# Kernel tuning notes

Hardware: AMD Instinct MI355X
Metric: run time of the kernel (lower is better)

The kernel has to match this reference:

```python
import jax, jax.numpy as jnp
import numpy as np

B, W, H, I, L = 64, 4096, 128, 128, 2


def setup_inputs() -> dict:
    key = jax.random.key(0)
    ks = jax.random.split(key, 16)
    f = lambda k, s: jax.random.normal(k, s, dtype=jnp.float32) * 0.05
    return dict(
        input=f(ks[0], (B, 1, I)),
        h0=f(ks[1], (L, B, H)),
        c0=f(ks[2], (L, B, H)),
        encoder_output=f(ks[3], (B, W, H)),
        att_W=f(ks[4], (1, 2 * H)), att_b=f(ks[5], (1,)),
        inp_W=f(ks[6], (I, H + I)), inp_b=f(ks[7], (I,)),
        W_ih0=f(ks[8], (4 * H, I)), W_hh0=f(ks[9], (4 * H, H)),
        b_ih0=f(ks[10], (4 * H,)), b_hh0=f(ks[11], (4 * H,)),
        W_ih1=f(ks[12], (4 * H, H)), W_hh1=f(ks[13], (4 * H, H)),
        b_ih1=f(ks[14], (4 * H,)), b_hh1=f(ks[15], (4 * H,)),
    )


def _lstm_cell(x, h, c, W_ih, W_hh, b_ih, b_hh):
    # PyTorch gate order: i, f, g, o
    gates = x @ W_ih.T + h @ W_hh.T + b_ih + b_hh
    i, f, g, o = jnp.split(gates, 4, axis=-1)
    c_new = jax.nn.sigmoid(f) * c + jax.nn.sigmoid(i) * jnp.tanh(g)
    h_new = jax.nn.sigmoid(o) * jnp.tanh(c_new)
    return h_new, c_new


def reference(input, h0, c0, encoder_output, att_W, att_b, inp_W, inp_b,
              W_ih0, W_hh0, b_ih0, b_hh0, W_ih1, W_hh1, b_ih1, b_hh1):
    att_state = h0[-1] * c0[-1]                       # (B, H)
    # att_line over concat(enc_word, att_state): split the (1, 2H) weight.
    wa_enc, wa_st = att_W[0, :H], att_W[0, H:]
    scores = encoder_output @ wa_enc + (att_state @ wa_st + att_b[0])[:, None]  # (B, W)
    # Faithful to original: a leading zeros column is prepended, then
    # softmax is taken over [:, 0:-1] -> keeps the zero column, drops the
    # LAST word's score.
    zero_col = jnp.zeros((scores.shape[0], 1), scores.dtype)
    full = jnp.concatenate([zero_col, scores], axis=1)  # (B, W+1)
    weight = jax.nn.softmax(full[:, :-1], axis=1)        # (B, W)
    x = jnp.einsum('bw,bwh->bh', weight, encoder_output)  # (B, H)
    xin = jnp.concatenate([x, input[:, 0, :]], axis=1) @ inp_W.T + inp_b  # (B, I)
    # 2-layer LSTM, single time step (eval mode -> inter-layer dropout off)
    h1, c1 = _lstm_cell(xin, h0[0], c0[0], W_ih0, W_hh0, b_ih0, b_hh0)
    h2, c2 = _lstm_cell(h1, h0[1], c0[1], W_ih1, W_hh1, b_ih1, b_hh1)
    output = h2[:, None, :]                              # (B, 1, H)
    return output, jnp.stack([h1, h2]), jnp.stack([c1, c2])
```

## Files before the change

### kernel.cpp

```cpp
#include <hip/hip_runtime.h>

#define BB 64
#define WW 4096
#define HH 128
#define NCHUNK 32
#define CROWS 128
#define PSTRIDE 132

__device__ inline float sigmoidf(float x) { return 1.0f / (1.0f + expf(-x)); }

__global__ void fused_attention(const float* __restrict__ enc,
                                const float* __restrict__ h0,
                                const float* __restrict__ c0,
                                const float* __restrict__ attW,
                                const float* __restrict__ attb,
                                float* __restrict__ partials) {
    __shared__ float s_wa[128];
    __shared__ float s_red[128];
    __shared__ float s_sc[CROWS];
    __shared__ float racc[16 * 128];
    __shared__ float s_bias, s_m, s_l;

    const int t = threadIdx.x;
    const int b = blockIdx.x >> 5;
    const int chunk = blockIdx.x & 31;
    const int w0 = chunk * CROWS;

    if (t < 128) {
        s_wa[t] = attW[t];
        float hv = h0[BB * HH + b * HH + t];
        float cv = c0[BB * HH + b * HH + t];
        s_red[t] = hv * cv * attW[HH + t];
    }
    __syncthreads();
    for (int s = 64; s > 0; s >>= 1) {
        if (t < s) s_red[t] += s_red[t + s];
        __syncthreads();
    }
    if (t == 0) s_bias = s_red[0] + attb[0];
    __syncthreads();
    const float bias = s_bias;

    const int seg = t & 15;
    const int rg  = t >> 4;
    float wseg[8];
#pragma unroll
    for (int j = 0; j < 8; j++) wseg[j] = s_wa[seg * 8 + j];

#pragma unroll
    for (int pass = 0; pass < 8; pass++) {
        const int r = pass * 16 + rg;
        const size_t w = (size_t)w0 + r;
        const float4* p = (const float4*)(enc + ((size_t)b * WW + w) * HH + seg * 8);
        float4 a = p[0], c = p[1];
        float d = a.x * wseg[0] + a.y * wseg[1] + a.z * wseg[2] + a.w * wseg[3]
                + c.x * wseg[4] + c.y * wseg[5] + c.z * wseg[6] + c.w * wseg[7];
        d += __shfl_xor(d, 8, 16);
        d += __shfl_xor(d, 4, 16);
        d += __shfl_xor(d, 2, 16);
        d += __shfl_xor(d, 1, 16);
        if (seg == 0) s_sc[r] = (w == WW - 1) ? -1e30f : (d + bias);
    }
    __syncthreads();

    if (t < 64) s_red[t] = fmaxf(s_sc[t], s_sc[t + 64]);
    __syncthreads();
    for (int s = 32; s > 0; s >>= 1) {
        if (t < s) s_red[t] = fmaxf(s_red[t], s_red[t + s]);
        __syncthreads();
    }
    if (t == 0) s_m = s_red[0];
    __syncthreads();
    const float m = s_m;

    if (t < 128) s_sc[t] = expf(s_sc[t] - m);
    __syncthreads();
    if (t < 64) s_red[t] = s_sc[t] + s_sc[t + 64];
    __syncthreads();
    for (int s = 32; s > 0; s >>= 1) {
        if (t < s) s_red[t] += s_red[t + s];
        __syncthreads();
    }
    if (t == 0) s_l = s_red[0];

    const int wsub = t >> 4;
    float acc8[8];
#pragma unroll
    for (int j = 0; j < 8; j++) acc8[j] = 0.f;
#pragma unroll
    for (int pass = 0; pass < 8; pass++) {
        const int r = pass * 16 + wsub;
        const size_t w = (size_t)w0 + r;
        if (w + 1 < WW) {
            const float pw = s_sc[r];
            const float4* p = (const float4*)(enc + ((size_t)b * WW + w + 1) * HH + seg * 8);
            float4 a = p[0], c = p[1];
            acc8[0] += pw * a.x; acc8[1] += pw * a.y;
            acc8[2] += pw * a.z; acc8[3] += pw * a.w;
            acc8[4] += pw * c.x; acc8[5] += pw * c.y;
            acc8[6] += pw * c.z; acc8[7] += pw * c.w;
        }
    }
#pragma unroll
    for (int j = 0; j < 8; j++) racc[wsub * 128 + seg * 8 + j] = acc8[j];
    __syncthreads();

    float* out = partials + (size_t)(b * NCHUNK + chunk) * PSTRIDE;
    if (t < 128) {
        float s = 0.f;
#pragma unroll
        for (int w2 = 0; w2 < 16; w2++) s += racc[w2 * 128 + t];
        out[t] = s;
    }
    if (t == 128) out[128] = m;
    if (t == 129) out[129] = s_l;
}

__global__ void tail_kernel(const float* __restrict__ partials,
                            const float* __restrict__ enc,
                            const float* __restrict__ input,
                            const float* __restrict__ inpW,
                            const float* __restrict__ inpb,
                            const float* __restrict__ Wih0,
                            const float* __restrict__ Whh0,
                            const float* __restrict__ bih0,
                            const float* __restrict__ bhh0,
                            const float* __restrict__ Wih1,
                            const float* __restrict__ Whh1,
                            const float* __restrict__ bih1,
                            const float* __restrict__ bhh1,
                            const float* __restrict__ h0,
                            const float* __restrict__ c0,
                            float* __restrict__ out) {
    __shared__ float lm[NCHUNK], llv[NCHUNK], ls[NCHUNK];
    __shared__ float sM, sL;
    __shared__ float xc[256];
    __shared__ float sxv[128];
    __shared__ float shv[128];
    __shared__ float sh1[128];
    __shared__ float shv2[128];
    __shared__ float gates[512];

    const int b = blockIdx.x;
    const int t = threadIdx.x;

    if (t < NCHUNK) {
        const float* pp = partials + (size_t)(b * NCHUNK + t) * PSTRIDE;
        lm[t] = pp[128];
        llv[t] = pp[129];
    }
    __syncthreads();
    if (t == 0) {
        float M = 0.0f;
        for (int c = 0; c < NCHUNK; c++) M = fmaxf(M, lm[c]);
        float L = expf(-M);
        for (int c = 0; c < NCHUNK; c++) {
            float s = expf(lm[c] - M);
            ls[c] = s;
            L += s * llv[c];
        }
        sM = M; sL = L;
    }
    __syncthreads();

    if (t < 128) {
        float xv = expf(-sM) * enc[(size_t)b * WW * HH + t];
        for (int c = 0; c < NCHUNK; c++)
            xv += ls[c] * partials[(size_t)(b * NCHUNK + c) * PSTRIDE + t];
        xc[t] = xv / sL;
        xc[128 + t] = input[b * HH + t];
    }
    __syncthreads();

    if (t < 128) {
        float a = inpb[t];
        const float4* wr = (const float4*)(inpW + (size_t)t * 256);
#pragma unroll
        for (int k = 0; k < 64; k++) {
            float4 w4 = wr[k];
            a += xc[4 * k] * w4.x + xc[4 * k + 1] * w4.y
               + xc[4 * k + 2] * w4.z + xc[4 * k + 3] * w4.w;
        }
        sxv[t] = a;
        shv[t] = h0[b * HH + t];
        shv2[t] = h0[BB * HH + b * HH + t];
    }
    __syncthreads();

    {
        float g = bih0[t] + bhh0[t];
        const float4* wi = (const float4*)(Wih0 + (size_t)t * 128);
        const float4* wh = (const float4*)(Whh0 + (size_t)t * 128);
#pragma unroll
        for (int k = 0; k < 32; k++) {
            float4 a = wi[k], c = wh[k];
            g += sxv[4 * k] * a.x + sxv[4 * k + 1] * a.y + sxv[4 * k + 2] * a.z + sxv[4 * k + 3] * a.w
               + shv[4 * k] * c.x + shv[4 * k + 1] * c.y + shv[4 * k + 2] * c.z + shv[4 * k + 3] * c.w;
        }
        gates[t] = g;
    }
    __syncthreads();
    if (t < 128) {
        float ig = sigmoidf(gates[t]);
        float fg = sigmoidf(gates[128 + t]);
        float gg = tanhf(gates[256 + t]);
        float og = sigmoidf(gates[384 + t]);
        float cn = fg * c0[b * HH + t] + ig * gg;
        float hn = og * tanhf(cn);
        out[8192 + b * HH + t] = hn;
        out[24576 + b * HH + t] = cn;
        sh1[t] = hn;
    }
    __syncthreads();

    {
        float g = bih1[t] + bhh1[t];
        const float4* wi = (const float4*)(Wih1 + (size_t)t * 128);
        const float4* wh = (const float4*)(Whh1 + (size_t)t * 128);
#pragma unroll
        for (int k = 0; k < 32; k++) {
            float4 a = wi[k], c = wh[k];
            g += sh1[4 * k] * a.x + sh1[4 * k + 1] * a.y + sh1[4 * k + 2] * a.z + sh1[4 * k + 3] * a.w
               + shv2[4 * k] * c.x + shv2[4 * k + 1] * c.y + shv2[4 * k + 2] * c.z + shv2[4 * k + 3] * c.w;
        }
        gates[t] = g;
    }
    __syncthreads();
    if (t < 128) {
        float ig = sigmoidf(gates[t]);
        float fg = sigmoidf(gates[128 + t]);
        float gg = tanhf(gates[256 + t]);
        float og = sigmoidf(gates[384 + t]);
        float cn = fg * c0[BB * HH + b * HH + t] + ig * gg;
        float hn = og * tanhf(cn);
        out[b * HH + t] = hn;
        out[16384 + b * HH + t] = hn;
        out[32768 + b * HH + t] = cn;
    }
}

extern "C" void kernel_launch(void* const* d_in, const int* in_sizes, int n_in,
                              void* d_out, int out_size, void* d_ws, size_t ws_size,
                              hipStream_t stream) {
    const float* input = (const float*)d_in[0];
    const float* h0    = (const float*)d_in[1];
    const float* c0    = (const float*)d_in[2];
    const float* enc   = (const float*)d_in[3];
    const float* attW  = (const float*)d_in[4];
    const float* attb  = (const float*)d_in[5];
    const float* inpW  = (const float*)d_in[6];
    const float* inpb  = (const float*)d_in[7];
    const float* Wih0  = (const float*)d_in[8];
    const float* Whh0  = (const float*)d_in[9];
    const float* bih0  = (const float*)d_in[10];
    const float* bhh0  = (const float*)d_in[11];
    const float* Wih1  = (const float*)d_in[12];
    const float* Whh1  = (const float*)d_in[13];
    const float* bih1  = (const float*)d_in[14];
    const float* bhh1  = (const float*)d_in[15];

    float* partials = (float*)d_ws;

    fused_attention<<<BB * NCHUNK, 256, 0, stream>>>(enc, h0, c0, attW, attb, partials);
    tail_kernel<<<BB, 512, 0, stream>>>(partials, enc, input, inpW, inpb,
                                        Wih0, Whh0, bih0, bhh0,
                                        Wih1, Whh1, bih1, bhh1,
                                        h0, c0, (float*)d_out);
}
```

Measured before the change: 285.6 us.

## Keep encoder rows in registers and re-index softmax weights to avoid second read

Result: faster. 272.9 us (-4.5%).

```diff
diff --git a/kernel.cpp b/kernel.cpp
--- a/kernel.cpp
+++ b/kernel.cpp
@@ -18,8 +18,9 @@
     __shared__ float s_wa[128];
     __shared__ float s_red[128];
     __shared__ float s_sc[CROWS];
+    __shared__ float s_p[CROWS];
     __shared__ float racc[16 * 128];
-    __shared__ float s_bias, s_m, s_l;
+    __shared__ float s_bias, s_m, s_extra;
 
     const int t = threadIdx.x;
     const int b = blockIdx.x >> 5;
@@ -47,11 +48,26 @@
 #pragma unroll
     for (int j = 0; j < 8; j++) wseg[j] = s_wa[seg * 8 + j];
 
+    float4 ra[8], rc[8];
 #pragma unroll
     for (int pass = 0; pass < 8; pass++) {
         const int r = pass * 16 + rg;
-        const size_t w = (size_t)w0 + r;
-        const float4* p = (const float4*)(enc + ((size_t)b * WW + w) * HH + seg * 8);
+        const float4* p = (const float4*)(enc + ((size_t)b * WW + w0 + r) * HH + seg * 8);
+        ra[pass] = p[0];
+        rc[pass] = p[1];
+        float d = ra[pass].x * wseg[0] + ra[pass].y * wseg[1]
+                + ra[pass].z * wseg[2] + ra[pass].w * wseg[3]
+                + rc[pass].x * wseg[4] + rc[pass].y * wseg[5]
+                + rc[pass].z * wseg[6] + rc[pass].w * wseg[7];
+        d += __shfl_xor(d, 8, 16);
+        d += __shfl_xor(d, 4, 16);
+        d += __shfl_xor(d, 2, 16);
+        d += __shfl_xor(d, 1, 16);
+        if (seg == 0) s_sc[r] = d + bias;
+    }
+
+    if (chunk > 0 && t < 16) {
+        const float4* p = (const float4*)(enc + ((size_t)b * WW + w0 - 1) * HH + t * 8);
         float4 a = p[0], c = p[1];
         float d = a.x * wseg[0] + a.y * wseg[1] + a.z * wseg[2] + a.w * wseg[3]
                 + c.x * wseg[4] + c.y * wseg[5] + c.z * wseg[6] + c.w * wseg[7];
@@ -59,11 +75,19 @@
         d += __shfl_xor(d, 4, 16);
         d += __shfl_xor(d, 2, 16);
         d += __shfl_xor(d, 1, 16);
-        if (seg == 0) s_sc[r] = (w == WW - 1) ? -1e30f : (d + bias);
-    }
-    __syncthreads();
-
-    if (t < 64) s_red[t] = fmaxf(s_sc[t], s_sc[t + 64]);
+        if (t == 0) s_extra = d + bias;
+    }
+    __syncthreads();
+
+    if (t < 128) {
+        float v;
+        if (t == 0) v = (chunk > 0) ? s_extra : -1e30f;
+        else        v = s_sc[t - 1];
+        s_p[t] = v;
+    }
+    __syncthreads();
+
+    if (t < 64) s_red[t] = fmaxf(s_p[t], s_p[t + 64]);
     __syncthreads();
     for (int s = 32; s > 0; s >>= 1) {
         if (t < s) s_red[t] = fmaxf(s_red[t], s_red[t + s]);
@@ -73,36 +97,29 @@
     __syncthreads();
     const float m = s_m;
 
-    if (t < 128) s_sc[t] = expf(s_sc[t] - m);
-    __syncthreads();
-    if (t < 64) s_red[t] = s_sc[t] + s_sc[t + 64];
+    if (t < 128) s_p[t] = expf(s_p[t] - m);
+    __syncthreads();
+    if (t < 64) s_red[t] = s_p[t] + s_p[t + 64];
     __syncthreads();
     for (int s = 32; s > 0; s >>= 1) {
         if (t < s) s_red[t] += s_red[t + s];
         __syncthreads();
     }
-    if (t == 0) s_l = s_red[0];
-
-    const int wsub = t >> 4;
+
     float acc8[8];
 #pragma unroll
     for (int j = 0; j < 8; j++) acc8[j] = 0.f;
 #pragma unroll
     for (int pass = 0; pass < 8; pass++) {
-        const int r = pass * 16 + wsub;
-        const size_t w = (size_t)w0 + r;
-        if (w + 1 < WW) {
-            const float pw = s_sc[r];
-            const float4* p = (const float4*)(enc + ((size_t)b * WW + w + 1) * HH + seg * 8);
-            float4 a = p[0], c = p[1];
-            acc8[0] += pw * a.x; acc8[1] += pw * a.y;
-            acc8[2] += pw * a.z; acc8[3] += pw * a.w;
-            acc8[4] += pw * c.x; acc8[5] += pw * c.y;
-            acc8[6] += pw * c.z; acc8[7] += pw * c.w;
-        }
-    }
-#pragma unroll
-    for (int j = 0; j < 8; j++) racc[wsub * 128 + seg * 8 + j] = acc8[j];
+        const int r = pass * 16 + rg;
+        const float pw = s_p[r];
+        acc8[0] += pw * ra[pass].x; acc8[1] += pw * ra[pass].y;
+        acc8[2] += pw * ra[pass].z; acc8[3] += pw * ra[pass].w;
+        acc8[4] += pw * rc[pass].x; acc8[5] += pw * rc[pass].y;
+        acc8[6] += pw * rc[pass].z; acc8[7] += pw * rc[pass].w;
+    }
+#pragma unroll
+    for (int j = 0; j < 8; j++) racc[rg * 128 + seg * 8 + j] = acc8[j];
     __syncthreads();
 
     float* out = partials + (size_t)(b * NCHUNK + chunk) * PSTRIDE;
@@ -113,7 +130,7 @@
         out[t] = s;
     }
     if (t == 128) out[128] = m;
-    if (t == 129) out[129] = s_l;
+    if (t == 129) out[129] = s_red[0];
 }
 
 __global__ void tail_kernel(const float* __restrict__ partials,
```
